# Performance work log

Measured on AMD Instinct MI355X. Metric: run time of the kernel, lower is better.

Reference implementation:

```python
import jax, jax.numpy as jnp
import numpy as np

ROPE_THETA = 500000.0


def apply_rope(x, position_ids):
    # x: (B, H, S, hd), position_ids: (B, S)
    hd = x.shape[-1]
    inv_freq = 1.0 / (ROPE_THETA ** (jnp.arange(0, hd, 2, dtype=x.dtype) / hd))  # (hd/2,)
    freqs = position_ids.astype(x.dtype)[:, :, None] * inv_freq  # (B, S, hd/2)
    sin = jnp.sin(freqs)[:, None, :, :]  # (B, 1, S, hd/2)
    cos = jnp.cos(freqs)[:, None, :, :]
    x1 = x[..., ::2]
    x2 = x[..., 1::2]
    even = x1 * cos - x2 * sin
    odd = x2 * cos + x1 * sin
    # interleave even/odd back: stack on a new trailing axis then flatten
    return jnp.stack([even, odd], axis=-1).reshape(x.shape)


def setup_inputs() -> dict:
    key = jax.random.key(0)
    k_x, k_q, k_k, k_v, k_o = jax.random.split(key, 5)
    B, S, D = 2, 2048, 2048
    H, H_kv = 32, 8
    hd = D // H
    x = jax.random.normal(k_x, (B, S, D), dtype=jnp.float32)
    position_ids = jnp.broadcast_to(jnp.arange(S, dtype=jnp.int64)[None, :], (B, S))
    scale = 0.02
    Wq = jax.random.normal(k_q, (D, H * hd), dtype=jnp.float32) * scale
    Wk = jax.random.normal(k_k, (D, H_kv * hd), dtype=jnp.float32) * scale
    Wv = jax.random.normal(k_v, (D, H_kv * hd), dtype=jnp.float32) * scale
    Wo = jax.random.normal(k_o, (D, D), dtype=jnp.float32) * scale
    return {"x": x, "position_ids": position_ids, "Wq": Wq, "Wk": Wk, "Wv": Wv, "Wo": Wo}


def reference(x, position_ids, Wq, Wk, Wv, Wo):
    B, S, D = x.shape
    H, H_kv = 32, 8
    hd = D // H
    G = H // H_kv  # query heads per kv head

    q = (x @ Wq).reshape(B, S, H, hd).transpose(0, 2, 1, 3)        # (B, H, S, hd)
    k = (x @ Wk).reshape(B, S, H_kv, hd).transpose(0, 2, 1, 3)     # (B, H_kv, S, hd)
    v = (x @ Wv).reshape(B, S, H_kv, hd).transpose(0, 2, 1, 3)

    q = apply_rope(q, position_ids)
    k = apply_rope(k, position_ids)

    # GQA: group query heads (B, H_kv, G, S, hd); repeat_interleave maps head h -> kv head h // G
    qg = q.reshape(B, H_kv, G, S, hd)
    scores = jnp.einsum("bkgsh,bkth->bkgst", qg, k) / jnp.sqrt(jnp.asarray(hd, x.dtype))

    causal = jnp.triu(jnp.ones((S, S), dtype=bool), 1)  # True = masked
    scores = jnp.where(causal, jnp.asarray(-jnp.inf, scores.dtype), scores)

    attn = jax.nn.softmax(scores, axis=-1)  # (B, H_kv, G, S, S)
    z = jnp.einsum("bkgst,bkth->bkgsh", attn, v)  # (B, H_kv, G, S, hd)
    z = z.reshape(B, H, S, hd).transpose(0, 2, 1, 3).reshape(B, S, D)
    return z @ Wo
```

## Files before the change

kernel.cpp:

```cpp
#include <hip/hip_runtime.h>
#include <hip/hip_bf16.h>


#define S_LEN 2048
#define DIM   2048
#define NH    32
#define NKV   8
#define HD    64
#define BS    4096
#define NQKV  3072
#define LL(x) ((long long)(x))

typedef __bf16 bf16x8 __attribute__((ext_vector_type(8)));
typedef float  f32x4  __attribute__((ext_vector_type(4)));

__device__ __forceinline__ unsigned short bfb(float f) {
  __hip_bfloat16 h = __float2bfloat16(f);
  return *reinterpret_cast<unsigned short*>(&h);
}

__device__ __forceinline__ unsigned cvtpk(float lo, float hi) {
  unsigned u;
  asm("v_cvt_pk_bf16_f32 %0, %1, %2" : "=v"(u) : "v"(lo), "v"(hi));
  return u;
}

__device__ __forceinline__ void gload16(const void* g, void* l) {
  __builtin_amdgcn_global_load_lds(
      (const __attribute__((address_space(1))) void*)g,
      (__attribute__((address_space(3))) void*)l, 16, 0, 0);
}

__global__ void k_rope_tab(float* __restrict__ tab) {
  int i = blockIdx.x * 256 + threadIdx.x;
  if (i >= S_LEN * 32) return;
  int s = i >> 5, f = i & 31;
  double inv = pow(500000.0, -2.0 * (double)f / 64.0);
  double fr = (double)s * inv;
  tab[2 * i]     = (float)cos(fr);
  tab[2 * i + 1] = (float)sin(fr);
}

__global__ void k_cast4(const float* __restrict__ in, unsigned short* __restrict__ out, int n4) {
  int i = blockIdx.x * 256 + threadIdx.x;
  if (i >= n4) return;
  float4 v = ((const float4*)in)[i];
  ushort4 o;
  o.x = bfb(v.x); o.y = bfb(v.y); o.z = bfb(v.z); o.w = bfb(v.w);
  ((ushort4*)out)[i] = o;
}

__global__ void k_tcast(const float* __restrict__ in, unsigned short* __restrict__ out,
                        int K, int N) {
  __shared__ float tile[32][33];
  int n0 = blockIdx.x * 32, k0 = blockIdx.y * 32;
  int tx = threadIdx.x, ty = threadIdx.y;
#pragma unroll
  for (int r = 0; r < 32; r += 8) tile[ty + r][tx] = in[LL(k0 + ty + r) * N + n0 + tx];
  __syncthreads();
#pragma unroll
  for (int r = 0; r < 32; r += 8) out[LL(n0 + ty + r) * K + k0 + tx] = bfb(tile[tx][ty + r]);
}

__global__ void k_vtrans(const unsigned short* __restrict__ vbuf, unsigned short* __restrict__ vt) {
  __shared__ __align__(16) unsigned short tile[64][72];
  int s0 = blockIdx.x * 64;
  int bh = blockIdx.y;
  int b = bh >> 3, kvh = bh & 7;
  int t = threadIdx.x;
#pragma unroll
  for (int c = t; c < 512; c += 256) {
    int s = c >> 3, seg = c & 7;
    *(uint4*)&tile[s][seg * 8] =
        *(const uint4*)(vbuf + LL(b * S_LEN + s0 + s) * (NKV * HD) + kvh * HD + seg * 8);
  }
  __syncthreads();
#pragma unroll
  for (int c = t; c < 512; c += 256) {
    int d = c >> 3, sseg = c & 7;
    ushort4 x0, x1;
    unsigned short* xp = (unsigned short*)&x0;
#pragma unroll
    for (int j = 0; j < 4; j++) xp[j] = tile[sseg * 8 + j][d];
    unsigned short* yp = (unsigned short*)&x1;
#pragma unroll
    for (int j = 0; j < 4; j++) yp[j] = tile[sseg * 8 + 4 + j][d];
    uint4 o;
    o.x = ((unsigned*)&x0)[0]; o.y = ((unsigned*)&x0)[1];
    o.z = ((unsigned*)&x1)[0]; o.w = ((unsigned*)&x1)[1];
    *(uint4*)(vt + (LL(bh) * HD + d) * S_LEN + s0 + sseg * 8) = o;
  }
}

template <int MODE>
__global__ __launch_bounds__(256, 2) void k_gemm(
    const unsigned short* __restrict__ A, const unsigned short* __restrict__ Bt,
    void* __restrict__ Cout, int M, int N, int K,
    const float* __restrict__ tab, unsigned short* __restrict__ qbuf,
    unsigned short* __restrict__ kbuf, unsigned short* __restrict__ vbuf) {
  __shared__ __align__(16) unsigned short As[128 * 32];
  __shared__ __align__(16) unsigned short Bs[128 * 32];
  int t = threadIdx.x;
  int lane = t & 63, w = t >> 6;
  int wr = w >> 1, wc = w & 1;
  int g = lane >> 4, r = lane & 15;
  int gx = gridDim.x;
  int nwg = gx * gridDim.y;
  int lin = blockIdx.y * gx + blockIdx.x;
  int cpx = nwg >> 3;
  int swz = (lin & 7) * cpx + (lin >> 3);
  int bx = swz % gx, by = swz / gx;
  long long rowBase = LL(by) * 128;
  long long colBase = LL(bx) * 128;

  f32x4 acc[4][4] = {};

  int c0 = t, c1 = t + 256;
  const unsigned short* ag0 = A + (rowBase + (c0 >> 2)) * K + (c0 & 3) * 8;
  const unsigned short* ag1 = A + (rowBase + (c1 >> 2)) * K + (c1 & 3) * 8;
  const unsigned short* bg0 = Bt + (colBase + (c0 >> 2)) * K + (c0 & 3) * 8;
  const unsigned short* bg1 = Bt + (colBase + (c1 >> 2)) * K + (c1 & 3) * 8;
  char* lA0 = (char*)As + c0 * 16; char* lA1 = (char*)As + c1 * 16;
  char* lB0 = (char*)Bs + c0 * 16; char* lB1 = (char*)Bs + c1 * 16;

  for (int kt = 0; kt < K; kt += 32) {
    __syncthreads();
    gload16(ag0 + kt, lA0);
    gload16(ag1 + kt, lA1);
    gload16(bg0 + kt, lB0);
    gload16(bg1 + kt, lB1);
    __syncthreads();

    bf16x8 af[4], bfr[4];
#pragma unroll
    for (int m = 0; m < 4; m++)
      af[m] = *(const bf16x8*)(const void*)(As + (wr * 64 + m * 16 + r) * 32 + g * 8);
#pragma unroll
    for (int n = 0; n < 4; n++)
      bfr[n] = *(const bf16x8*)(const void*)(Bs + (wc * 64 + n * 16 + r) * 32 + g * 8);
#pragma unroll
    for (int m = 0; m < 4; m++)
#pragma unroll
      for (int n = 0; n < 4; n++)
        acc[m][n] = __builtin_amdgcn_mfma_f32_16x16x32_bf16(af[m], bfr[n], acc[m][n], 0, 0, 0);
  }

  if (MODE == 0) {
#pragma unroll
    for (int m = 0; m < 4; m++)
#pragma unroll
      for (int n = 0; n < 4; n++) {
        long long row0 = rowBase + wr * 64 + m * 16 + g * 4;
        long long col = colBase + wc * 64 + n * 16 + r;
#pragma unroll
        for (int j = 0; j < 4; j++)
          ((float*)Cout)[(row0 + j) * N + col] = acc[m][n][j];
      }
  } else {
#pragma unroll
    for (int n = 0; n < 4; n++) {
      int gc0 = (int)colBase + wc * 64 + n * 16;
      int gc = gc0 + r;
      unsigned short* dst; int dcol, dstride; float scale; bool rope;
      if (gc0 < 2048)      { dst = qbuf; dcol = gc;        dstride = DIM; scale = 0.18033688f; rope = true; }
      else if (gc0 < 2560) { dst = kbuf; dcol = gc - 2048; dstride = 512; scale = 1.0f;        rope = true; }
      else                 { dst = vbuf; dcol = gc - 2560; dstride = 512; scale = 1.0f;        rope = false; }
      int f = (gc & 63) >> 1;
      float sgn = (gc & 1) ? 1.f : -1.f;
#pragma unroll
      for (int m = 0; m < 4; m++) {
        long long row0 = rowBase + wr * 64 + m * 16 + g * 4;
#pragma unroll
        for (int j = 0; j < 4; j++) {
          float v = acc[m][n][j];
          float o;
          if (rope) {
            float part = __shfl_xor(v, 1);
            int s = (int)((row0 + j) & (S_LEN - 1));
            float cc = tab[(s * 32 + f) * 2], ss = tab[(s * 32 + f) * 2 + 1];
            o = (v * cc + sgn * part * ss) * scale;
          } else o = v;
          dst[(row0 + j) * dstride + dcol] = bfb(o);
        }
      }
    }
  }
}

__global__ __launch_bounds__(256, 4) void k_attn(
    const unsigned short* __restrict__ qb, const unsigned short* __restrict__ kb,
    const unsigned short* __restrict__ vt, unsigned short* __restrict__ zb) {
  int pair = blockIdx.x;
  int h = blockIdx.y, b = blockIdx.z;
  int kvh = h >> 2, bh = b * NKV + kvh;
  int t = threadIdx.x, lane = t & 63, w = t >> 6;
  int g = lane >> 4, r = lane & 15;
  int sw = (r & 7) * 8;

  __shared__ __align__(16) unsigned short Ks[2][64 * 64];
  __shared__ __align__(16) unsigned short Vs[2][64 * 64];
  __shared__ __align__(16) unsigned short Ps[4][16 * 64];

  unsigned short* Pw = Ps[w];

  int c0 = t, c1 = t + 256;
  const unsigned short* kg0 = kb + LL(b) * S_LEN * 512 + (c0 >> 3) * 512 + kvh * HD
                                 + (((c0 & 7) ^ ((c0 >> 3) & 7)) * 8);
  const unsigned short* kg1 = kb + LL(b) * S_LEN * 512 + (c1 >> 3) * 512 + kvh * HD
                                 + (((c1 & 7) ^ ((c1 >> 3) & 7)) * 8);
  const unsigned short* vg0 = vt + (LL(bh) * HD + (c0 >> 3)) * S_LEN
                                 + (((c0 & 7) ^ ((c0 >> 3) & 7)) * 8);
  const unsigned short* vg1 = vt + (LL(bh) * HD + (c1 >> 3)) * S_LEN
                                 + (((c1 & 7) ^ ((c1 >> 3) & 7)) * 8);

#define STAGE(bufi, kst_)                                              \
  {                                                                    \
    gload16(kg0 + LL(kst_) * 512, (char*)Ks[bufi] + c0 * 16);          \
    gload16(kg1 + LL(kst_) * 512, (char*)Ks[bufi] + c1 * 16);          \
    gload16(vg0 + (kst_), (char*)Vs[bufi] + c0 * 16);                  \
    gload16(vg1 + (kst_), (char*)Vs[bufi] + c1 * 16);                  \
  }

#pragma unroll 1
  for (int pass = 0; pass < 2; pass++) {
    int qt = pass ? (31 - pair) : pair;
    int qbase = qt * 64;
    int qglob = qbase + w * 16 + r;
    long long qrow = LL(b) * S_LEN + qglob;

    bf16x8 qf[2];
    qf[0] = *(const bf16x8*)(const void*)(qb + qrow * DIM + h * HD + g * 8);
    qf[1] = *(const bf16x8*)(const void*)(qb + qrow * DIM + h * HD + 32 + g * 8);

    f32x4 acc[4] = {};
    float mrun = -1e30f, lrun = 0.f;

    int nt = qt + 1;
    __syncthreads();
    STAGE(0, 0);
    for (int tt = 0; tt < nt; tt++) {
      int kst = tt * 64;
      int cur = tt & 1;
      if (tt + 1 < nt) {
        STAGE(cur ^ 1, kst + 64);
        asm volatile("s_waitcnt vmcnt(4)" ::: "memory");
      } else {
        asm volatile("s_waitcnt vmcnt(0)" ::: "memory");
      }
      __builtin_amdgcn_s_barrier();
      __builtin_amdgcn_sched_barrier(0);

      const unsigned short* Kc = Ks[cur];
      const unsigned short* Vc = Vs[cur];

      bf16x8 kfr[4][2];
#pragma unroll
      for (int nf = 0; nf < 4; nf++)
#pragma unroll
        for (int kd = 0; kd < 2; kd++)
          kfr[nf][kd] = *(const bf16x8*)(const void*)(
              Kc + (nf * 16 + r) * 64 + ((kd * 32 + g * 8) ^ sw));

      __builtin_amdgcn_s_setprio(1);
      f32x4 sc[4] = {};
#pragma unroll
      for (int nf = 0; nf < 4; nf++)
#pragma unroll
        for (int kd = 0; kd < 2; kd++)
          sc[nf] = __builtin_amdgcn_mfma_f32_16x16x32_bf16(
              kfr[nf][kd], qf[kd], sc[nf], 0, 0, 0);
      __builtin_amdgcn_s_setprio(0);

      if (tt == nt - 1) {
#pragma unroll
        for (int nf = 0; nf < 4; nf++)
#pragma unroll
          for (int j = 0; j < 4; j++)
            if (kst + nf * 16 + g * 4 + j > qglob) sc[nf][j] = -1e30f;
      }

      float pm = fmaxf(fmaxf(fmaxf(sc[0][0], sc[0][1]), fmaxf(sc[0][2], sc[0][3])),
                       fmaxf(fmaxf(sc[1][0], sc[1][1]), fmaxf(sc[1][2], sc[1][3])));
      pm = fmaxf(pm, fmaxf(fmaxf(fmaxf(sc[2][0], sc[2][1]), fmaxf(sc[2][2], sc[2][3])),
                           fmaxf(fmaxf(sc[3][0], sc[3][1]), fmaxf(sc[3][2], sc[3][3]))));
      pm = fmaxf(pm, __shfl_xor(pm, 16));
      pm = fmaxf(pm, __shfl_xor(pm, 32));
      if (__any(pm > mrun + 12.0f)) {
        float mnew = fmaxf(mrun, pm);
        float al = exp2f(mrun - mnew);
        mrun = mnew;
        lrun *= al;
#pragma unroll
        for (int d = 0; d < 4; d++) acc[d] *= al;
      }
      float ls = 0.f;
#pragma unroll
      for (int nf = 0; nf < 4; nf++) {
        float p0 = exp2f(sc[nf][0] - mrun);
        float p1 = exp2f(sc[nf][1] - mrun);
        float p2 = exp2f(sc[nf][2] - mrun);
        float p3 = exp2f(sc[nf][3] - mrun);
        ls += (p0 + p1) + (p2 + p3);
        uint2 u;
        u.x = cvtpk(p0, p1);
        u.y = cvtpk(p2, p3);
        *(uint2*)(void*)(Pw + r * 64 + ((nf * 16 + g * 4) ^ sw)) = u;
      }
      ls += __shfl_xor(ls, 16);
      ls += __shfl_xor(ls, 32);
      lrun += ls;

      asm volatile("s_waitcnt lgkmcnt(0)" ::: "memory");
      __builtin_amdgcn_sched_barrier(0);

      bf16x8 pf[2];
      pf[0] = *(const bf16x8*)(const void*)(Pw + r * 64 + ((g * 8) ^ sw));
      pf[1] = *(const bf16x8*)(const void*)(Pw + r * 64 + ((32 + g * 8) ^ sw));
      __builtin_amdgcn_s_setprio(1);
#pragma unroll
      for (int d = 0; d < 4; d++)
#pragma unroll
        for (int ks = 0; ks < 2; ks++) {
          bf16x8 vfr = *(const bf16x8*)(const void*)(
              Vc + (d * 16 + r) * 64 + ((ks * 32 + g * 8) ^ sw));
          acc[d] = __builtin_amdgcn_mfma_f32_16x16x32_bf16(
              vfr, pf[ks], acc[d], 0, 0, 0);
        }
      __builtin_amdgcn_s_setprio(0);

      __builtin_amdgcn_sched_barrier(0);
      __builtin_amdgcn_s_barrier();
    }

    float inv = 1.0f / lrun;
#pragma unroll
    for (int d = 0; d < 4; d++) {
      uint2 u;
      u.x = cvtpk(acc[d][0] * inv, acc[d][1] * inv);
      u.y = cvtpk(acc[d][2] * inv, acc[d][3] * inv);
      *(uint2*)(void*)(zb + qrow * DIM + h * HD + d * 16 + g * 4) = u;
    }
  }
#undef STAGE
}

extern "C" void kernel_launch(void* const* d_in, const int* in_sizes, int n_in,
                              void* d_out, int out_size, void* d_ws, size_t ws_size,
                              hipStream_t stream) {
  const float* x  = (const float*)d_in[0];
  const float* Wq = (const float*)d_in[2];
  const float* Wk = (const float*)d_in[3];
  const float* Wv = (const float*)d_in[4];
  const float* Wo = (const float*)d_in[5];
  float* out = (float*)d_out;

  char* wsb = (char*)d_ws;
  size_t off = 0;
  auto alloc = [&](size_t bytes) {
    void* p = wsb + off;
    off += (bytes + 255) & ~(size_t)255;
    return p;
  };
  float* tab            = (float*)alloc(LL(S_LEN) * 32 * 2 * 4);
  unsigned short* xb    = (unsigned short*)alloc(LL(BS) * DIM * 2);
  unsigned short* wqkvt = (unsigned short*)alloc(LL(NQKV) * DIM * 2);
  unsigned short* wot   = (unsigned short*)alloc(LL(DIM) * DIM * 2);
  unsigned short* qbuf  = (unsigned short*)alloc(LL(BS) * DIM * 2);
  unsigned short* kbuf  = (unsigned short*)alloc(LL(BS) * (NKV * HD) * 2);
  unsigned short* vbuf  = (unsigned short*)alloc(LL(BS) * (NKV * HD) * 2);
  unsigned short* vtb   = (unsigned short*)alloc(LL(2 * NKV) * HD * S_LEN * 2);
  unsigned short* zb    = (unsigned short*)alloc(LL(BS) * DIM * 2);

  k_rope_tab<<<(S_LEN * 32 + 255) / 256, 256, 0, stream>>>(tab);
  k_cast4<<<(BS * DIM / 4 + 255) / 256, 256, 0, stream>>>(x, xb, BS * DIM / 4);
  k_tcast<<<dim3(DIM / 32, DIM / 32), dim3(32, 8), 0, stream>>>(Wq, wqkvt, DIM, DIM);
  k_tcast<<<dim3(512 / 32, DIM / 32), dim3(32, 8), 0, stream>>>(Wk, wqkvt + LL(2048) * DIM, DIM, 512);
  k_tcast<<<dim3(512 / 32, DIM / 32), dim3(32, 8), 0, stream>>>(Wv, wqkvt + LL(2560) * DIM, DIM, 512);
  k_tcast<<<dim3(DIM / 32, DIM / 32), dim3(32, 8), 0, stream>>>(Wo, wot, DIM, DIM);

  k_gemm<2><<<dim3(NQKV / 128, BS / 128), 256, 0, stream>>>(
      xb, wqkvt, nullptr, BS, NQKV, DIM, tab, qbuf, kbuf, vbuf);

  k_vtrans<<<dim3(S_LEN / 64, 2 * NKV), 256, 0, stream>>>(vbuf, vtb);

  k_attn<<<dim3(16, NH, 2), 256, 0, stream>>>(qbuf, kbuf, vtb, zb);

  k_gemm<0><<<dim3(DIM / 128, BS / 128), 256, 0, stream>>>(
      zb, wot, out, BS, DIM, DIM, nullptr, nullptr, nullptr, nullptr);
}
```

Measured before the change: 230.3 us.

## Rework attention to 32x32x16 MFMA with 128-row query tiles and register P

The attention kernel moves from 16x16x32 to 32x32x16 bf16 MFMA, with each wave owning 32 query rows in a 128-row block tile. The grid halves and is remapped so that blocks sharing a KV head are adjacent. P is now built in registers through a cross-half-wave shuffle instead of a round trip through LDS, and K/V tiles past a wave's causal limit are skipped. The aim is to cut LDS traffic and instruction count per FLOP and to improve K/V cache reuse. In exchange, register pressure rises (launch bounds drop to 2) and some waves sit idle on the diagonal tiles.

```diff
diff --git a/kernel.cpp b/kernel.cpp
--- a/kernel.cpp
+++ b/kernel.cpp
@@ -13,6 +13,8 @@
 
 typedef __bf16 bf16x8 __attribute__((ext_vector_type(8)));
 typedef float  f32x4  __attribute__((ext_vector_type(4)));
+typedef float  f32x16 __attribute__((ext_vector_type(16)));
+typedef unsigned u32x4 __attribute__((ext_vector_type(4)));
 
 __device__ __forceinline__ unsigned short bfb(float f) {
   __hip_bfloat16 h = __float2bfloat16(f);
@@ -187,21 +189,24 @@
   }
 }
 
-__global__ __launch_bounds__(256, 4) void k_attn(
+__global__ __launch_bounds__(256, 2) void k_attn(
     const unsigned short* __restrict__ qb, const unsigned short* __restrict__ kb,
     const unsigned short* __restrict__ vt, unsigned short* __restrict__ zb) {
-  int pair = blockIdx.x;
-  int h = blockIdx.y, b = blockIdx.z;
-  int kvh = h >> 2, bh = b * NKV + kvh;
+  int lin = blockIdx.x + 8 * (blockIdx.y + 32 * blockIdx.z);
+  int kvh = lin & 7;
+  int idx = lin >> 3;
+  int b = idx >> 5;
+  int j = idx & 31;
+  int h = kvh * 4 + (j & 3);
+  int pair = j >> 2;
+  int bh = b * NKV + kvh;
+
   int t = threadIdx.x, lane = t & 63, w = t >> 6;
-  int g = lane >> 4, r = lane & 15;
-  int sw = (r & 7) * 8;
+  int l31 = lane & 31, hi = lane >> 5;
+  int sw = (l31 & 7) * 8;
 
   __shared__ __align__(16) unsigned short Ks[2][64 * 64];
   __shared__ __align__(16) unsigned short Vs[2][64 * 64];
-  __shared__ __align__(16) unsigned short Ps[4][16 * 64];
-
-  unsigned short* Pw = Ps[w];
 
   int c0 = t, c1 = t + 256;
   const unsigned short* kg0 = kb + LL(b) * S_LEN * 512 + (c0 >> 3) * 512 + kvh * HD
@@ -223,19 +228,20 @@
 
 #pragma unroll 1
   for (int pass = 0; pass < 2; pass++) {
-    int qt = pass ? (31 - pair) : pair;
-    int qbase = qt * 64;
-    int qglob = qbase + w * 16 + r;
-    long long qrow = LL(b) * S_LEN + qglob;
-
-    bf16x8 qf[2];
-    qf[0] = *(const bf16x8*)(const void*)(qb + qrow * DIM + h * HD + g * 8);
-    qf[1] = *(const bf16x8*)(const void*)(qb + qrow * DIM + h * HD + 32 + g * 8);
-
-    f32x4 acc[4] = {};
+    int st = pass ? (15 - pair) : pair;
+    int rowb = st * 128 + w * 32;
+    int qg = rowb + l31;
+    long long qrow = LL(b) * S_LEN + qg;
+
+    bf16x8 qf[4];
+#pragma unroll
+    for (int s = 0; s < 4; s++)
+      qf[s] = *(const bf16x8*)(const void*)(qb + qrow * DIM + h * HD + s * 16 + hi * 8);
+
+    f32x16 acc0 = {}, acc1 = {};
     float mrun = -1e30f, lrun = 0.f;
 
-    int nt = qt + 1;
+    int nt = 2 * st + 2;
     __syncthreads();
     STAGE(0, 0);
     for (int tt = 0; tt < nt; tt++) {
@@ -250,95 +256,117 @@
       __builtin_amdgcn_s_barrier();
       __builtin_amdgcn_sched_barrier(0);
 
-      const unsigned short* Kc = Ks[cur];
-      const unsigned short* Vc = Vs[cur];
-
-      bf16x8 kfr[4][2];
-#pragma unroll
-      for (int nf = 0; nf < 4; nf++)
-#pragma unroll
-        for (int kd = 0; kd < 2; kd++)
-          kfr[nf][kd] = *(const bf16x8*)(const void*)(
-              Kc + (nf * 16 + r) * 64 + ((kd * 32 + g * 8) ^ sw));
-
-      __builtin_amdgcn_s_setprio(1);
-      f32x4 sc[4] = {};
-#pragma unroll
-      for (int nf = 0; nf < 4; nf++)
-#pragma unroll
-        for (int kd = 0; kd < 2; kd++)
-          sc[nf] = __builtin_amdgcn_mfma_f32_16x16x32_bf16(
-              kfr[nf][kd], qf[kd], sc[nf], 0, 0, 0);
-      __builtin_amdgcn_s_setprio(0);
-
-      if (tt == nt - 1) {
-#pragma unroll
-        for (int nf = 0; nf < 4; nf++)
-#pragma unroll
-          for (int j = 0; j < 4; j++)
-            if (kst + nf * 16 + g * 4 + j > qglob) sc[nf][j] = -1e30f;
+      if (kst <= rowb + 31) {
+        const unsigned short* Kc = Ks[cur];
+        const unsigned short* Vc = Vs[cur];
+
+        bf16x8 kf[2][4];
+#pragma unroll
+        for (int kbi = 0; kbi < 2; kbi++)
+#pragma unroll
+          for (int s = 0; s < 4; s++)
+            kf[kbi][s] = *(const bf16x8*)(const void*)(
+                Kc + (kbi * 32 + l31) * 64 + ((s * 16 + hi * 8) ^ sw));
+
+        __builtin_amdgcn_s_setprio(1);
+        f32x16 sc0 = {}, sc1 = {};
+#pragma unroll
+        for (int s = 0; s < 4; s++) {
+          sc0 = __builtin_amdgcn_mfma_f32_32x32x16_bf16(kf[0][s], qf[s], sc0, 0, 0, 0);
+          sc1 = __builtin_amdgcn_mfma_f32_32x32x16_bf16(kf[1][s], qf[s], sc1, 0, 0, 0);
+        }
+        __builtin_amdgcn_s_setprio(0);
+
+        bf16x8 vf[8];
+#pragma unroll
+        for (int db = 0; db < 2; db++)
+#pragma unroll
+          for (int f = 0; f < 4; f++)
+            vf[db * 4 + f] = *(const bf16x8*)(const void*)(
+                Vc + (db * 32 + l31) * 64 + ((f * 16 + hi * 8) ^ sw));
+
+        if (kst + 63 > rowb) {
+#pragma unroll
+          for (int q = 0; q < 16; q++) {
+            int kl = (q & 3) + 8 * (q >> 2) + 4 * hi;
+            if (kst + kl > qg) sc0[q] = -1e30f;
+            if (kst + 32 + kl > qg) sc1[q] = -1e30f;
+          }
+        }
+
+        float pm = -1e30f;
+#pragma unroll
+        for (int q = 0; q < 16; q++) {
+          pm = fmaxf(pm, sc0[q]);
+          pm = fmaxf(pm, sc1[q]);
+        }
+        pm = fmaxf(pm, __shfl_xor(pm, 32));
+        if (__any(pm > mrun + 12.0f)) {
+          float mnew = fmaxf(mrun, pm);
+          float al = exp2f(mrun - mnew);
+          mrun = mnew;
+          lrun *= al;
+          acc0 *= al;
+          acc1 *= al;
+        }
+        f32x16 pv0, pv1;
+        float ls = 0.f;
+#pragma unroll
+        for (int q = 0; q < 16; q++) {
+          pv0[q] = exp2f(sc0[q] - mrun);
+          pv1[q] = exp2f(sc1[q] - mrun);
+          ls += pv0[q] + pv1[q];
+        }
+        lrun += ls + __shfl_xor(ls, 32);
+
+        bf16x8 pfr[4];
+#pragma unroll
+        for (int f = 0; f < 4; f++) {
+          int qb_ = (f & 1) * 8;
+          float e0, e1, e2, e3, e4, e5, e6, e7;
+          if (f < 2) {
+            e0 = pv0[qb_ + 0]; e1 = pv0[qb_ + 1]; e2 = pv0[qb_ + 2]; e3 = pv0[qb_ + 3];
+            e4 = pv0[qb_ + 4]; e5 = pv0[qb_ + 5]; e6 = pv0[qb_ + 6]; e7 = pv0[qb_ + 7];
+          } else {
+            e0 = pv1[qb_ + 0]; e1 = pv1[qb_ + 1]; e2 = pv1[qb_ + 2]; e3 = pv1[qb_ + 3];
+            e4 = pv1[qb_ + 4]; e5 = pv1[qb_ + 5]; e6 = pv1[qb_ + 6]; e7 = pv1[qb_ + 7];
+          }
+          unsigned a0 = cvtpk(e0, e1), a1 = cvtpk(e2, e3);
+          unsigned b0 = cvtpk(e4, e5), b1 = cvtpk(e6, e7);
+          unsigned y0 = __shfl_xor(hi ? a0 : b0, 32);
+          unsigned y1 = __shfl_xor(hi ? a1 : b1, 32);
+          u32x4 uu;
+          uu[0] = hi ? y0 : a0;
+          uu[1] = hi ? y1 : a1;
+          uu[2] = hi ? b0 : y0;
+          uu[3] = hi ? b1 : y1;
+          pfr[f] = *(bf16x8*)&uu;
+        }
+
+        __builtin_amdgcn_s_setprio(1);
+#pragma unroll
+        for (int f = 0; f < 4; f++) {
+          acc0 = __builtin_amdgcn_mfma_f32_32x32x16_bf16(vf[f],     pfr[f], acc0, 0, 0, 0);
+          acc1 = __builtin_amdgcn_mfma_f32_32x32x16_bf16(vf[4 + f], pfr[f], acc1, 0, 0, 0);
+        }
+        __builtin_amdgcn_s_setprio(0);
       }
-
-      float pm = fmaxf(fmaxf(fmaxf(sc[0][0], sc[0][1]), fmaxf(sc[0][2], sc[0][3])),
-                       fmaxf(fmaxf(sc[1][0], sc[1][1]), fmaxf(sc[1][2], sc[1][3])));
-      pm = fmaxf(pm, fmaxf(fmaxf(fmaxf(sc[2][0], sc[2][1]), fmaxf(sc[2][2], sc[2][3])),
-                           fmaxf(fmaxf(sc[3][0], sc[3][1]), fmaxf(sc[3][2], sc[3][3]))));
-      pm = fmaxf(pm, __shfl_xor(pm, 16));
-      pm = fmaxf(pm, __shfl_xor(pm, 32));
-      if (__any(pm > mrun + 12.0f)) {
-        float mnew = fmaxf(mrun, pm);
-        float al = exp2f(mrun - mnew);
-        mrun = mnew;
-        lrun *= al;
-#pragma unroll
-        for (int d = 0; d < 4; d++) acc[d] *= al;
-      }
-      float ls = 0.f;
-#pragma unroll
-      for (int nf = 0; nf < 4; nf++) {
-        float p0 = exp2f(sc[nf][0] - mrun);
-        float p1 = exp2f(sc[nf][1] - mrun);
-        float p2 = exp2f(sc[nf][2] - mrun);
-        float p3 = exp2f(sc[nf][3] - mrun);
-        ls += (p0 + p1) + (p2 + p3);
-        uint2 u;
-        u.x = cvtpk(p0, p1);
-        u.y = cvtpk(p2, p3);
-        *(uint2*)(void*)(Pw + r * 64 + ((nf * 16 + g * 4) ^ sw)) = u;
-      }
-      ls += __shfl_xor(ls, 16);
-      ls += __shfl_xor(ls, 32);
-      lrun += ls;
-
-      asm volatile("s_waitcnt lgkmcnt(0)" ::: "memory");
-      __builtin_amdgcn_sched_barrier(0);
-
-      bf16x8 pf[2];
-      pf[0] = *(const bf16x8*)(const void*)(Pw + r * 64 + ((g * 8) ^ sw));
-      pf[1] = *(const bf16x8*)(const void*)(Pw + r * 64 + ((32 + g * 8) ^ sw));
-      __builtin_amdgcn_s_setprio(1);
-#pragma unroll
-      for (int d = 0; d < 4; d++)
-#pragma unroll
-        for (int ks = 0; ks < 2; ks++) {
-          bf16x8 vfr = *(const bf16x8*)(const void*)(
-              Vc + (d * 16 + r) * 64 + ((ks * 32 + g * 8) ^ sw));
-          acc[d] = __builtin_amdgcn_mfma_f32_16x16x32_bf16(
-              vfr, pf[ks], acc[d], 0, 0, 0);
-        }
-      __builtin_amdgcn_s_setprio(0);
 
       __builtin_amdgcn_sched_barrier(0);
       __builtin_amdgcn_s_barrier();
     }
 
-    float inv = 1.0f / lrun;
-#pragma unroll
-    for (int d = 0; d < 4; d++) {
+    float invl = 1.0f / lrun;
+#pragma unroll
+    for (int q4 = 0; q4 < 4; q4++) {
       uint2 u;
-      u.x = cvtpk(acc[d][0] * inv, acc[d][1] * inv);
-      u.y = cvtpk(acc[d][2] * inv, acc[d][3] * inv);
-      *(uint2*)(void*)(zb + qrow * DIM + h * HD + d * 16 + g * 4) = u;
+      u.x = cvtpk(acc0[q4 * 4 + 0] * invl, acc0[q4 * 4 + 1] * invl);
+      u.y = cvtpk(acc0[q4 * 4 + 2] * invl, acc0[q4 * 4 + 3] * invl);
+      *(uint2*)(void*)(zb + qrow * DIM + h * HD + 8 * q4 + 4 * hi) = u;
+      uint2 v;
+      v.x = cvtpk(acc1[q4 * 4 + 0] * invl, acc1[q4 * 4 + 1] * invl);
+      v.y = cvtpk(acc1[q4 * 4 + 2] * invl, acc1[q4 * 4 + 3] * invl);
+      *(uint2*)(void*)(zb + qrow * DIM + h * HD + 32 + 8 * q4 + 4 * hi) = v;
     }
   }
 #undef STAGE
@@ -383,7 +411,7 @@
 
   k_vtrans<<<dim3(S_LEN / 64, 2 * NKV), 256, 0, stream>>>(vbuf, vtb);
 
-  k_attn<<<dim3(16, NH, 2), 256, 0, stream>>>(qbuf, kbuf, vtb, zb);
+  k_attn<<<dim3(8, NH, 2), 256, 0, stream>>>(qbuf, kbuf, vtb, zb);
 
   k_gemm<0><<<dim3(DIM / 128, BS / 128), 256, 0, stream>>>(
       zb, wot, out, BS, DIM, DIM, nullptr, nullptr, nullptr, nullptr);
```

After: 229.8 us. Within noise of the previous version (-0.2%).
